# Kernel tuning notes

Measured on AMD Instinct MI355X. Metric: run time of the kernel, lower is better.

## Reference

```python
import jax, jax.numpy as jnp
import numpy as np

N_NODES = 100000
N_EDGES = 1000000
IN_DIM = 64
HID = 64
OUT = 64
NEG_SLOPE = 0.2  # PyG GATConv default


def setup_inputs() -> dict:
    key = jax.random.key(0)
    ks = jax.random.split(key, 10)
    x = jax.random.normal(ks[0], (N_NODES, IN_DIM), dtype=jnp.float32)
    edge_index = jax.random.randint(ks[1], (2, N_EDGES), 0, N_NODES, dtype=jnp.int64)
    s = 1.0 / np.sqrt(IN_DIM)
    sh = 1.0 / np.sqrt(HID)
    W_src = jax.random.uniform(ks[2], (IN_DIM, HID), jnp.float32, -s, s)
    W_dst = jax.random.uniform(ks[3], (IN_DIM, HID), jnp.float32, -s, s)
    att_src = jax.random.uniform(ks[4], (HID,), jnp.float32, -sh, sh)
    att_dst = jax.random.uniform(ks[5], (HID,), jnp.float32, -sh, sh)
    bias = jnp.zeros((HID,), jnp.float32)
    W_lin = jax.random.uniform(ks[6], (HID, OUT), jnp.float32, -sh, sh)
    b_lin = jax.random.uniform(ks[7], (OUT,), jnp.float32, -sh, sh)
    return {"x": x, "edge_index": edge_index, "W_src": W_src, "W_dst": W_dst,
            "att_src": att_src, "att_dst": att_dst, "bias": bias,
            "W_lin": W_lin, "b_lin": b_lin}


def reference(x, edge_index, W_src, W_dst, att_src, att_dst, bias, W_lin, b_lin):
    src, tgt = edge_index[0], edge_index[1]
    # Bias-free linear projections (PyG GATConv with tuple in_channels)
    h_src = x @ W_src                      # [N, HID]
    h_dst = x @ W_dst                      # [N, HID]
    a_src = h_src @ att_src                # [N]
    a_dst = h_dst @ att_dst                # [N]
    # Per-edge attention logits: LeakyReLU(a_src[j] + a_dst[i])
    e = a_src[src] + a_dst[tgt]            # [E]
    e = jnp.where(e > 0, e, NEG_SLOPE * e)
    # Segment-softmax over incoming edges of each target node
    seg_max = jax.ops.segment_max(e, tgt, num_segments=N_NODES)  # [N]
    expw = jnp.exp(e - seg_max[tgt])                             # [E]
    denom = jax.ops.segment_sum(expw, tgt, num_segments=N_NODES)  # [N]
    alpha = expw / (denom[tgt] + 1e-16)                          # [E]
    # Scatter-aggregate weighted source features
    msgs = alpha[:, None] * h_src[src]                           # [E, HID]
    out = jax.ops.segment_sum(msgs, tgt, num_segments=N_NODES)   # [N, HID]
    out = out + bias
    # Final linear + ReLU
    return jax.nn.relu(out @ W_lin + b_lin)
```

## Files before the change

### kernel.cpp

```cpp
#include <hip/hip_runtime.h>
#include <hip/hip_fp16.h>
#include <math.h>

#define HID 64
#define CBITS 6
#define CSZ 64
#define MAXB 2048
#define CAP 832
#define CAPH 448
#define PB 896
#define MSB 256

__device__ __forceinline__ float4 f4fma(float a, const float4 b, float4 c) {
    c.x = fmaf(a, b.x, c.x); c.y = fmaf(a, b.y, c.y);
    c.z = fmaf(a, b.z, c.z); c.w = fmaf(a, b.w, c.w);
    return c;
}

__global__ void init_kernel(const float* __restrict__ W_dst,
                            const float* __restrict__ att_dst,
                            float* __restrict__ vdst,
                            int* __restrict__ gcursor, int nbc) {
    if (blockIdx.x == 0 && threadIdx.x < HID) {
        int k = threadIdx.x;
        float acc = 0.0f;
#pragma unroll 8
        for (int h = 0; h < HID; ++h) acc = fmaf(W_dst[k * HID + h], att_dst[h], acc);
        vdst[k] = acc;
    }
    int stride = gridDim.x * blockDim.x;
    for (int i = blockIdx.x * blockDim.x + threadIdx.x; i < nbc; i += stride)
        gcursor[i] = i * CAP;
}

__global__ void __launch_bounds__(256)
mid_kernel(const float* __restrict__ x,
           const float* __restrict__ W_src,
           const float* __restrict__ att_src,
           const float* __restrict__ vdst,
           __half* __restrict__ h_half,
           float* __restrict__ a_src,
           float* __restrict__ a_dst, int N,
           const int* __restrict__ src, const int* __restrict__ tgt,
           int* __restrict__ gcursor, int* __restrict__ rec, int E, int nbc) {
    __shared__ __align__(16) char smraw[25088];
    const int t = threadIdx.x;

    if (blockIdx.x < PB) {
        float4* Ws4  = (float4*)smraw;
        float4* att4 = Ws4 + HID * 16;
        float4* vd4  = att4 + 16;
        float*  xs   = (float*)(vd4 + 16);

        for (int i = t; i < HID * 16; i += 256) Ws4[i] = ((const float4*)W_src)[i];
        if (t < 16) {
            att4[t] = ((const float4*)att_src)[t];
            vd4[t]  = ((const float4*)vdst)[t];
        }

        const int g0 = t >> 4;
        const int s = t & 15;
        const float4* x4 = (const float4*)x;
        uint2* h2 = (uint2*)h_half;
        float4* xs4 = (float4*)xs;

        for (int base = blockIdx.x * 32; base < N; base += PB * 32) {
            __syncthreads();
#pragma unroll
            for (int u = 0; u < 2; ++u) {
                int f = t + u * 256;
                int node = base + (f >> 4);
                xs4[f] = (node < N) ? x4[node * 16 + (f & 15)]
                                    : make_float4(0, 0, 0, 0);
            }
            __syncthreads();

            const float*  xr0  = xs + g0 * HID;
            const float*  xr1  = xs + (g0 + 16) * HID;
            const float4* xr0v = (const float4*)xr0;
            const float4* xr1v = (const float4*)xr1;

            float4 acc0 = make_float4(0, 0, 0, 0);
            float4 acc1 = make_float4(0, 0, 0, 0);
#pragma unroll 2
            for (int k4 = 0; k4 < 16; ++k4) {
                float4 xv0 = xr0v[k4];
                float4 xv1 = xr1v[k4];
                float4 wa = Ws4[(4 * k4 + 0) * 16 + s];
                float4 wb = Ws4[(4 * k4 + 1) * 16 + s];
                float4 wc = Ws4[(4 * k4 + 2) * 16 + s];
                float4 wd = Ws4[(4 * k4 + 3) * 16 + s];
                acc0 = f4fma(xv0.x, wa, acc0); acc1 = f4fma(xv1.x, wa, acc1);
                acc0 = f4fma(xv0.y, wb, acc0); acc1 = f4fma(xv1.y, wb, acc1);
                acc0 = f4fma(xv0.z, wc, acc0); acc1 = f4fma(xv1.z, wc, acc1);
                acc0 = f4fma(xv0.w, wd, acc0); acc1 = f4fma(xv1.w, wd, acc1);
            }

            float4 av = att4[s], qv = vd4[s];
            float p0 = acc0.x * av.x + acc0.y * av.y + acc0.z * av.z + acc0.w * av.w;
            float p1 = acc1.x * av.x + acc1.y * av.y + acc1.z * av.z + acc1.w * av.w;
            float q0 = xr0[4 * s] * qv.x + xr0[4 * s + 1] * qv.y +
                       xr0[4 * s + 2] * qv.z + xr0[4 * s + 3] * qv.w;
            float q1 = xr1[4 * s] * qv.x + xr1[4 * s + 1] * qv.y +
                       xr1[4 * s + 2] * qv.z + xr1[4 * s + 3] * qv.w;
#pragma unroll
            for (int off = 1; off < 16; off <<= 1) {
                p0 += __shfl_xor(p0, off, 64);
                p1 += __shfl_xor(p1, off, 64);
                q0 += __shfl_xor(q0, off, 64);
                q1 += __shfl_xor(q1, off, 64);
            }

            int n0 = base + g0, n1 = base + g0 + 16;
            if (n0 < N) {
                __half2 lo = __float22half2_rn(make_float2(acc0.x, acc0.y));
                __half2 hi = __float22half2_rn(make_float2(acc0.z, acc0.w));
                uint2 pk; pk.x = *(unsigned*)&lo; pk.y = *(unsigned*)&hi;
                h2[n0 * 16 + s] = pk;
                if (s == 0) { a_src[n0] = p0; a_dst[n0] = q0; }
            }
            if (n1 < N) {
                __half2 lo = __float22half2_rn(make_float2(acc1.x, acc1.y));
                __half2 hi = __float22half2_rn(make_float2(acc1.z, acc1.w));
                uint2 pk; pk.x = *(unsigned*)&lo; pk.y = *(unsigned*)&hi;
                h2[n1 * 16 + s] = pk;
                if (s == 0) { a_src[n1] = p1; a_dst[n1] = q1; }
            }
        }
    } else {
        int* lh = (int*)smraw;
        const int bid = blockIdx.x - PB;

        for (int i = t; i < nbc; i += 256) lh[i] = 0;
        __syncthreads();
        int chunk = (E + MSB - 1) / MSB;
        int e0 = bid * chunk;
        int e1 = min(E, e0 + chunk);
        for (int e = e0 + t; e < e1; e += 256)
            atomicAdd(&lh[tgt[e] >> CBITS], 1);
        __syncthreads();
        for (int i = t; i < nbc; i += 256)
            if (lh[i]) lh[i] = atomicAdd(&gcursor[i], lh[i]);
        __syncthreads();
        for (int e = e0 + t; e < e1; e += 256) {
            int s = src[e], tg = tgt[e];
            int bi = tg >> CBITS;
            int pos = atomicAdd(&lh[bi], 1);
            if (pos < (bi + 1) * CAP)
                rec[pos] = (s << CBITS) | (tg & (CSZ - 1));
        }
    }
}

__global__ void __launch_bounds__(256)
sort_gather_kernel(const int* __restrict__ gcursor, const int* __restrict__ rec,
                   const __half* __restrict__ h_half,
                   const float* __restrict__ a_src, const float* __restrict__ a_dst,
                   const float* __restrict__ bias,
                   const float* __restrict__ W_lin, const float* __restrict__ b_lin,
                   float* __restrict__ out, int N) {
    __shared__ float4 Wl4[HID * 16];
    __shared__ float4 bs4[16], bl4[16];
    __shared__ int ssort[CAPH];
    __shared__ unsigned short wgt[CAPH];
    __shared__ float adl[32];
    __shared__ int hist[32];
    __shared__ int loff[33];
    __shared__ int cur[32];
    __shared__ int sd[32];

    const int t = threadIdx.x;
    for (int i = t; i < HID * 16; i += 256) Wl4[i] = ((const float4*)W_lin)[i];
    if (t < 16) {
        bs4[t] = ((const float4*)bias)[t];
        bl4[t] = ((const float4*)b_lin)[t];
    }

    const int bk = blockIdx.x >> 1;
    const int half = blockIdx.x & 1;
    const int node0 = (bk << CBITS) + half * 32;
    const int nn = min(32, N - node0);
    const int beg = bk * CAP;
    int cnt = gcursor[bk] - beg;
    if (cnt > CAP) cnt = CAP;

    if (t < 32) {
        hist[t] = 0;
        adl[t] = (node0 + t < N) ? a_dst[node0 + t] : 0.0f;
    }
    __syncthreads();
    for (int j = t; j < cnt; j += 256) {
        int tl = rec[beg + j] & (CSZ - 1);
        if ((tl >> 5) == half) atomicAdd(&hist[tl & 31], 1);
    }
    __syncthreads();
    if (t < 32) sd[t] = hist[t];
    __syncthreads();
    for (int off = 1; off < 32; off <<= 1) {
        int v = (t < 32 && t >= off) ? sd[t - off] : 0;
        __syncthreads();
        if (t < 32) sd[t] += v;
        __syncthreads();
    }
    if (t < 32) {
        int e = sd[t] - hist[t];
        loff[t] = e; cur[t] = e;
        if (t == 31) loff[32] = min(sd[31], CAPH);
    }
    __syncthreads();
    for (int j = t; j < cnt; j += 256) {
        int r = rec[beg + j];
        int tl = r & (CSZ - 1);
        if ((tl >> 5) == half) {
            int sidx = r >> CBITS;
            float v = a_src[sidx] + adl[tl & 31];
            v = (v > 0.0f) ? v : 0.2f * v;
            float w = __expf(v);
            int pos = atomicAdd(&cur[tl & 31], 1);
            if (pos < CAPH) {
                ssort[pos] = sidx;
                wgt[pos] = __half_as_ushort(__float2half_rn(w));
            }
        }
    }
    __syncthreads();

    const int lane = t & 63;
    const int w = t >> 6;
    const int g = lane >> 4;
    const int s = lane & 15;
    const int gbase = g << 4;
    const uint2* h2 = (const uint2*)h_half;
    float4* out4 = (float4*)out;

#pragma unroll 1
    for (int r2 = 0; r2 < 2; ++r2) {
        int nloc = w * 8 + r2 * 4 + g;
        int n = node0 + nloc;
        bool act = (nloc < nn);
        int jb = min(loff[nloc], CAPH);
        int je = min(loff[nloc + 1], CAPH);

        float4 acc = make_float4(0, 0, 0, 0);
        float dsum = 0.0f;
        int j = jb;
        for (; j + 4 <= je; j += 4) {
            int s0 = ssort[j], s1 = ssort[j + 1], s2 = ssort[j + 2], s3 = ssort[j + 3];
            float w0 = __half2float(__ushort_as_half(wgt[j]));
            float w1 = __half2float(__ushort_as_half(wgt[j + 1]));
            float w2 = __half2float(__ushort_as_half(wgt[j + 2]));
            float w3 = __half2float(__ushort_as_half(wgt[j + 3]));
            uint2 r0 = h2[s0 * 16 + s];
            uint2 r1 = h2[s1 * 16 + s];
            uint2 r2v = h2[s2 * 16 + s];
            uint2 r3 = h2[s3 * 16 + s];
            dsum += (w0 + w1) + (w2 + w3);
            float2 f0a = __half22float2(*(const __half2*)&r0.x);
            float2 f0b = __half22float2(*(const __half2*)&r0.y);
            float2 f1a = __half22float2(*(const __half2*)&r1.x);
            float2 f1b = __half22float2(*(const __half2*)&r1.y);
            float2 f2a = __half22float2(*(const __half2*)&r2v.x);
            float2 f2b = __half22float2(*(const __half2*)&r2v.y);
            float2 f3a = __half22float2(*(const __half2*)&r3.x);
            float2 f3b = __half22float2(*(const __half2*)&r3.y);
            acc.x = fmaf(w0, f0a.x, fmaf(w1, f1a.x, fmaf(w2, f2a.x, fmaf(w3, f3a.x, acc.x))));
            acc.y = fmaf(w0, f0a.y, fmaf(w1, f1a.y, fmaf(w2, f2a.y, fmaf(w3, f3a.y, acc.y))));
            acc.z = fmaf(w0, f0b.x, fmaf(w1, f1b.x, fmaf(w2, f2b.x, fmaf(w3, f3b.x, acc.z))));
            acc.w = fmaf(w0, f0b.y, fmaf(w1, f1b.y, fmaf(w2, f2b.y, fmaf(w3, f3b.y, acc.w))));
        }
        for (; j < je; ++j) {
            int s0 = ssort[j];
            float w0 = __half2float(__ushort_as_half(wgt[j]));
            uint2 r0 = h2[s0 * 16 + s];
            dsum += w0;
            float2 f0a = __half22float2(*(const __half2*)&r0.x);
            float2 f0b = __half22float2(*(const __half2*)&r0.y);
            acc.x = fmaf(w0, f0a.x, acc.x);
            acc.y = fmaf(w0, f0a.y, acc.y);
            acc.z = fmaf(w0, f0b.x, acc.z);
            acc.w = fmaf(w0, f0b.y, acc.w);
        }

        float inv = 1.0f / (dsum + 1e-16f);
        float4 bsv = bs4[s];
        float4 r;
        r.x = fmaf(acc.x, inv, bsv.x);
        r.y = fmaf(acc.y, inv, bsv.y);
        r.z = fmaf(acc.z, inv, bsv.z);
        r.w = fmaf(acc.w, inv, bsv.w);

        float4 o = bl4[s];
#pragma unroll 4
        for (int ks = 0; ks < 16; ++ks) {
            float rx = __shfl(r.x, gbase + ks, 64);
            float ry = __shfl(r.y, gbase + ks, 64);
            float rz = __shfl(r.z, gbase + ks, 64);
            float rw = __shfl(r.w, gbase + ks, 64);
            o = f4fma(rx, Wl4[(4 * ks + 0) * 16 + s], o);
            o = f4fma(ry, Wl4[(4 * ks + 1) * 16 + s], o);
            o = f4fma(rz, Wl4[(4 * ks + 2) * 16 + s], o);
            o = f4fma(rw, Wl4[(4 * ks + 3) * 16 + s], o);
        }

        if (act) {
            float4 res;
            res.x = o.x > 0.0f ? o.x : 0.0f;
            res.y = o.y > 0.0f ? o.y : 0.0f;
            res.z = o.z > 0.0f ? o.z : 0.0f;
            res.w = o.w > 0.0f ? o.w : 0.0f;
            out4[n * 16 + s] = res;
        }
    }
}

extern "C" void kernel_launch(void* const* d_in, const int* in_sizes, int n_in,
                              void* d_out, int out_size, void* d_ws, size_t ws_size,
                              hipStream_t stream) {
    const float* x       = (const float*)d_in[0];
    const int*   edge    = (const int*)d_in[1];
    const float* W_src   = (const float*)d_in[2];
    const float* W_dst   = (const float*)d_in[3];
    const float* att_src = (const float*)d_in[4];
    const float* att_dst = (const float*)d_in[5];
    const float* bias    = (const float*)d_in[6];
    const float* W_lin   = (const float*)d_in[7];
    const float* b_lin   = (const float*)d_in[8];
    float* out = (float*)d_out;

    const int N = in_sizes[0] / HID;
    const int E = in_sizes[1] / 2;
    const int* src = edge;
    const int* tgt = edge + E;
    const int nbc = (N + CSZ - 1) / CSZ;

    __half* h_half  = (__half*)d_ws;
    float*  a_src   = (float*)(h_half + (size_t)N * HID);
    float*  a_dst   = a_src + N;
    float*  vdst    = a_dst + N;
    int*    gcursor = (int*)(vdst + 64);
    int*    rec     = gcursor + MAXB;

    init_kernel<<<8, 256, 0, stream>>>(W_dst, att_dst, vdst, gcursor, nbc);
    mid_kernel<<<PB + MSB, 256, 0, stream>>>(x, W_src, att_src, vdst, h_half,
                                             a_src, a_dst, N,
                                             src, tgt, gcursor, rec, E, nbc);
    sort_gather_kernel<<<nbc * 2, 256, 0, stream>>>(gcursor, rec, h_half, a_src, a_dst,
                                                    bias, W_lin, b_lin, out, N);
}
```

Measured before the change: 179.0 us.

## Compute attention weights in gather loop and unroll edge loop by eight

Stops precomputing per-edge exp weights into shared memory during the sort pass. Each of the 16 lanes in a group now recomputes the weight from a_src and a_dst inside the gather loop, which is unrolled to 8 edges to put more loads in flight. Dropping the weight array frees shared memory, so CAPH grows and launch bounds ask for 8 blocks per CU. The cost is redundant a_src loads and exp work across the 16 lanes of each group, plus the exp is now in full precision rather than stored as half.

```diff
diff --git a/kernel.cpp b/kernel.cpp
--- a/kernel.cpp
+++ b/kernel.cpp
@@ -7,7 +7,7 @@
 #define CSZ 64
 #define MAXB 2048
 #define CAP 832
-#define CAPH 448
+#define CAPH 576
 #define PB 896
 #define MSB 256
 
@@ -152,7 +152,7 @@
     }
 }
 
-__global__ void __launch_bounds__(256)
+__global__ void __launch_bounds__(256, 8)
 sort_gather_kernel(const int* __restrict__ gcursor, const int* __restrict__ rec,
                    const __half* __restrict__ h_half,
                    const float* __restrict__ a_src, const float* __restrict__ a_dst,
@@ -162,8 +162,6 @@
     __shared__ float4 Wl4[HID * 16];
     __shared__ float4 bs4[16], bl4[16];
     __shared__ int ssort[CAPH];
-    __shared__ unsigned short wgt[CAPH];
-    __shared__ float adl[32];
     __shared__ int hist[32];
     __shared__ int loff[33];
     __shared__ int cur[32];
@@ -184,10 +182,7 @@
     int cnt = gcursor[bk] - beg;
     if (cnt > CAP) cnt = CAP;
 
-    if (t < 32) {
-        hist[t] = 0;
-        adl[t] = (node0 + t < N) ? a_dst[node0 + t] : 0.0f;
-    }
+    if (t < 32) hist[t] = 0;
     __syncthreads();
     for (int j = t; j < cnt; j += 256) {
         int tl = rec[beg + j] & (CSZ - 1);
@@ -212,15 +207,8 @@
         int r = rec[beg + j];
         int tl = r & (CSZ - 1);
         if ((tl >> 5) == half) {
-            int sidx = r >> CBITS;
-            float v = a_src[sidx] + adl[tl & 31];
-            v = (v > 0.0f) ? v : 0.2f * v;
-            float w = __expf(v);
             int pos = atomicAdd(&cur[tl & 31], 1);
-            if (pos < CAPH) {
-                ssort[pos] = sidx;
-                wgt[pos] = __half_as_ushort(__float2half_rn(w));
-            }
+            if (pos < CAPH) ssort[pos] = r >> CBITS;
         }
     }
     __syncthreads();
@@ -238,40 +226,46 @@
         int nloc = w * 8 + r2 * 4 + g;
         int n = node0 + nloc;
         bool act = (nloc < nn);
+        float adn = act ? a_dst[n] : 0.0f;
         int jb = min(loff[nloc], CAPH);
         int je = min(loff[nloc + 1], CAPH);
 
         float4 acc = make_float4(0, 0, 0, 0);
         float dsum = 0.0f;
         int j = jb;
-        for (; j + 4 <= je; j += 4) {
-            int s0 = ssort[j], s1 = ssort[j + 1], s2 = ssort[j + 2], s3 = ssort[j + 3];
-            float w0 = __half2float(__ushort_as_half(wgt[j]));
-            float w1 = __half2float(__ushort_as_half(wgt[j + 1]));
-            float w2 = __half2float(__ushort_as_half(wgt[j + 2]));
-            float w3 = __half2float(__ushort_as_half(wgt[j + 3]));
-            uint2 r0 = h2[s0 * 16 + s];
-            uint2 r1 = h2[s1 * 16 + s];
-            uint2 r2v = h2[s2 * 16 + s];
-            uint2 r3 = h2[s3 * 16 + s];
-            dsum += (w0 + w1) + (w2 + w3);
-            float2 f0a = __half22float2(*(const __half2*)&r0.x);
-            float2 f0b = __half22float2(*(const __half2*)&r0.y);
-            float2 f1a = __half22float2(*(const __half2*)&r1.x);
-            float2 f1b = __half22float2(*(const __half2*)&r1.y);
-            float2 f2a = __half22float2(*(const __half2*)&r2v.x);
-            float2 f2b = __half22float2(*(const __half2*)&r2v.y);
-            float2 f3a = __half22float2(*(const __half2*)&r3.x);
-            float2 f3b = __half22float2(*(const __half2*)&r3.y);
-            acc.x = fmaf(w0, f0a.x, fmaf(w1, f1a.x, fmaf(w2, f2a.x, fmaf(w3, f3a.x, acc.x))));
-            acc.y = fmaf(w0, f0a.y, fmaf(w1, f1a.y, fmaf(w2, f2a.y, fmaf(w3, f3a.y, acc.y))));
-            acc.z = fmaf(w0, f0b.x, fmaf(w1, f1b.x, fmaf(w2, f2b.x, fmaf(w3, f3b.x, acc.z))));
-            acc.w = fmaf(w0, f0b.y, fmaf(w1, f1b.y, fmaf(w2, f2b.y, fmaf(w3, f3b.y, acc.w))));
+        for (; j + 8 <= je; j += 8) {
+            int   sl[8];
+            uint2 hr[8];
+            float wv[8];
+#pragma unroll
+            for (int u = 0; u < 8; ++u) sl[u] = ssort[j + u];
+#pragma unroll
+            for (int u = 0; u < 8; ++u) hr[u] = h2[sl[u] * 16 + s];
+#pragma unroll
+            for (int u = 0; u < 8; ++u) wv[u] = a_src[sl[u]] + adn;
+#pragma unroll
+            for (int u = 0; u < 8; ++u) {
+                float v = wv[u];
+                v = (v > 0.0f) ? v : 0.2f * v;
+                wv[u] = __expf(v);
+            }
+#pragma unroll
+            for (int u = 0; u < 8; ++u) {
+                dsum += wv[u];
+                float2 fa = __half22float2(*(const __half2*)&hr[u].x);
+                float2 fb = __half22float2(*(const __half2*)&hr[u].y);
+                acc.x = fmaf(wv[u], fa.x, acc.x);
+                acc.y = fmaf(wv[u], fa.y, acc.y);
+                acc.z = fmaf(wv[u], fb.x, acc.z);
+                acc.w = fmaf(wv[u], fb.y, acc.w);
+            }
         }
         for (; j < je; ++j) {
             int s0 = ssort[j];
-            float w0 = __half2float(__ushort_as_half(wgt[j]));
             uint2 r0 = h2[s0 * 16 + s];
+            float v0 = a_src[s0] + adn;
+            v0 = (v0 > 0.0f) ? v0 : 0.2f * v0;
+            float w0 = __expf(v0);
             dsum += w0;
             float2 f0a = __half22float2(*(const __half2*)&r0.x);
             float2 f0b = __half22float2(*(const __half2*)&r0.y);
```

After: 169.7 us. 1.05x faster.
